# Kernel tuning notes

Measured on AMD Instinct MI355X. Metric: run time of the kernel, lower is better.

## Reference

```python
import jax, jax.numpy as jnp
import numpy as np

N, E, C, H, R, L, ED = 10000, 160000, 512, 4, 8, 2, 768
O = C // H  # out_channels per head = 128
NEG_SLOPE = 0.2
LN_EPS = 1e-5


def setup_inputs() -> dict:
    key = jax.random.key(0)
    ks = jax.random.split(key, 14)
    s = 0.05
    return {
        "x": jax.random.normal(ks[0], (N, C), jnp.float32),
        "edge_index": jax.random.randint(ks[1], (2, E), 0, N, dtype=jnp.int64),
        "edge_type": jax.random.randint(ks[2], (E,), 0, R, dtype=jnp.int64),
        "edge_repre": jax.random.normal(ks[3], (E, ED), jnp.float32),
        # per-layer RGATConv params (num_layers clones)
        "weight": jax.random.normal(ks[4], (L, R, C, C), jnp.float32) * s,   # [L,R,in,heads*out]
        "q": jax.random.normal(ks[5], (L, C, H), jnp.float32) * s,            # [L,heads*out,heads*dim], dim=1
        "k": jax.random.normal(ks[6], (L, C, H), jnp.float32) * s,
        "e": jax.random.normal(ks[7], (L, C, H), jnp.float32) * s,
        "w_edge": jax.random.normal(ks[8], (L, ED, C), jnp.float32) * s,      # lin_edge (no bias)
        "conv_bias": jnp.zeros((L, C), jnp.float32),
        # shared LayerNorm + FFN
        "ln_gamma": jnp.ones((C,), jnp.float32),
        "ln_beta": jnp.zeros((C,), jnp.float32),
        "ff1_w": jax.random.normal(ks[9], (C, 2 * C), jnp.float32) * s,
        "ff1_b": jnp.zeros((2 * C,), jnp.float32),
        "ff2_w": jax.random.normal(ks[10], (2 * C, C), jnp.float32) * s,
        "ff2_b": jnp.zeros((C,), jnp.float32),
    }


def _layer_norm(x, g, b):
    m = jnp.mean(x, axis=-1, keepdims=True)
    v = jnp.mean(jnp.square(x - m), axis=-1, keepdims=True)
    return g * (x - m) * jax.lax.rsqrt(v + LN_EPS) + b


def _rgat_conv(x, src, dst, etype, eattr, W, q, k, e, We, bias):
    n = x.shape[0]
    # relation-specific transform of all nodes once: [N,R,C]
    xw = jnp.einsum('nc,rcd->nrd', x, W)
    outi = xw[dst, etype]            # [E,C] target feats under edge's relation
    outj = xw[src, etype]            # [E,C] source feats under edge's relation
    qi = outi @ q                     # [E,H]
    kj = outj @ k                     # [E,H]
    ae = (eattr @ We) @ e             # [E,H]
    alpha = jax.nn.leaky_relu(qi + kj + ae, NEG_SLOPE)
    # across-relation segment softmax over incoming edges of each target node
    amax = jax.ops.segment_max(alpha, dst, num_segments=n)
    ex = jnp.exp(alpha - amax[dst])
    denom = jax.ops.segment_sum(ex, dst, num_segments=n)
    alpha = ex / (denom[dst] + 1e-16)
    msg = alpha[:, :, None] * outj.reshape(-1, H, O)          # [E,H,O]
    out = jax.ops.segment_sum(msg, dst, num_segments=n)       # [N,H,O]
    return out.reshape(n, H * O) + bias


def reference(x, edge_index, edge_type, edge_repre, weight, q, k, e, w_edge,
              conv_bias, ln_gamma, ln_beta, ff1_w, ff1_b, ff2_w, ff2_b):
    src, dst = edge_index[0], edge_index[1]
    enc_emb = x
    for l in range(L):
        x = _rgat_conv(x, src, dst, edge_type, edge_repre, weight[l], q[l],
                       k[l], e[l], w_edge[l], conv_bias[l]) + x
    x = _layer_norm(x + enc_emb, ln_gamma, ln_beta)
    x = jax.nn.relu(x @ ff1_w + ff1_b) @ ff2_w + ff2_b + x
    x = _layer_norm(x, ln_gamma, ln_beta)
    return x + enc_emb
```

## Files before the change

### kernel.cpp

```cpp
#include <hip/hip_runtime.h>
#include <hip/hip_bf16.h>

#define NN 10000
#define EE 160000
#define CC 512
#define HH 4
#define RR 8
#define LL 2
#define EDD 768
#define OO 128

typedef __attribute__((ext_vector_type(8))) short bf16x8;
typedef __attribute__((ext_vector_type(4))) float f32x4;

__global__ void trg_hist(const int* __restrict__ ei, int* __restrict__ deg) {
  int e = blockIdx.x * 256 + threadIdx.x;
  if (e < EE) atomicAdd(&deg[ei[EE + e]], 1);
}

__global__ void trg_scan(const int* __restrict__ deg, int* __restrict__ offs,
                         int* __restrict__ cursor) {
  __shared__ int sp[256];
  int t = threadIdx.x;
  const int CHK = (NN + 255) / 256;
  int lo = t * CHK, hi = lo + CHK; if (hi > NN) hi = NN; if (lo > NN) lo = NN;
  int s = 0;
  for (int i = lo; i < hi; i++) s += deg[i];
  sp[t] = s;
  __syncthreads();
  if (t == 0) {
    int run = 0;
    for (int i = 0; i < 256; i++) { int v = sp[i]; sp[i] = run; run += v; }
  }
  __syncthreads();
  int run = sp[t];
  for (int i = lo; i < hi; i++) { offs[i] = run; cursor[i] = run; run += deg[i]; }
  if (t == 255) offs[NN] = run;
}

__global__ void trg_fill(const int* __restrict__ ei, int* __restrict__ cursor,
                         int* __restrict__ elist) {
  int e = blockIdx.x * 256 + threadIdx.x;
  if (e < EE) {
    int pos = atomicAdd(&cursor[ei[EE + e]], 1);
    elist[pos] = e;
  }
}

__global__ void trg_transpose(const float* __restrict__ in, __hip_bfloat16* __restrict__ out,
                              int P, int Q, long inStride, long outStride) {
  __shared__ float tile[32][33];
  int z = blockIdx.z;
  const float* inz = in + (long)z * inStride;
  __hip_bfloat16* outz = out + (long)z * outStride;
  int q0 = blockIdx.x * 32, p0 = blockIdx.y * 32;
  int tx = threadIdx.x, ty = threadIdx.y;
#pragma unroll
  for (int i = 0; i < 4; i++)
    tile[ty + i * 8][tx] = inz[(long)(p0 + ty + i * 8) * Q + q0 + tx];
  __syncthreads();
#pragma unroll
  for (int i = 0; i < 4; i++)
    outz[(long)(q0 + ty + i * 8) * P + p0 + tx] = __float2bfloat16(tile[tx][ty + i * 8]);
}

__global__ void trg_cast_bf16(const float* __restrict__ in, __hip_bfloat16* __restrict__ out, int n4) {
  int i = blockIdx.x * 256 + threadIdx.x;
  if (i >= n4) return;
  float4 v = ((const float4*)in)[i];
  union { ushort4 u; __hip_bfloat16 h[4]; } cv;
  cv.h[0] = __float2bfloat16(v.x); cv.h[1] = __float2bfloat16(v.y);
  cv.h[2] = __float2bfloat16(v.z); cv.h[3] = __float2bfloat16(v.w);
  ((ushort4*)out)[i] = cv.u;
}

__global__ void trg_me(const float* __restrict__ we, const float* __restrict__ ep,
                       float* __restrict__ Me) {
  int idx = blockIdx.x * 256 + threadIdx.x;
  if (idx >= LL * EDD * HH) return;
  int l = idx / (EDD * HH);
  int r = idx % (EDD * HH);
  int ed = r / HH, h = r % HH;
  const float* wr = we + ((long)l * EDD + ed) * CC;
  const float* ec = ep + (long)l * CC * HH + h;
  float acc = 0.f;
  for (int c = 0; c < CC; c++) acc += wr[c] * ec[c * HH];
  Me[idx] = acc;
}

__global__ void trg_qcat(const float* __restrict__ qp, const float* __restrict__ kp,
                         float* __restrict__ qcat) {
  int idx = blockIdx.x * 256 + threadIdx.x;
  if (idx >= LL * CC * 8) return;
  int l = idx / (CC * 8);
  int r = idx % (CC * 8);
  int c = r >> 3, j = r & 7;
  qcat[idx] = (j < 4) ? qp[((long)l * CC + c) * HH + j]
                      : kp[((long)l * CC + c) * HH + (j - 4)];
}

__global__ void trg_ae(const float* __restrict__ eattr, const float* __restrict__ Me,
                       float* __restrict__ AE) {
  __shared__ float sE[32 * 129];
  __shared__ float sM[128 * 8];
  int t = threadIdx.x;
  int e0 = blockIdx.x * 32;
  int el = t & 31, og = t >> 5;
  float acc = 0.f;
  for (int kc = 0; kc < 6; kc++) {
    __syncthreads();
    for (int idx = t; idx < 32 * 128; idx += 256) {
      int row = idx >> 7, col = idx & 127;
      sE[row * 129 + col] = eattr[(long)(e0 + row) * EDD + kc * 128 + col];
    }
    for (int idx = t; idx < 128 * 8; idx += 256) {
      int c = idx >> 3, o = idx & 7;
      int l = o >> 2, h = o & 3;
      sM[c * 8 + o] = Me[((long)l * EDD + kc * 128 + c) * 4 + h];
    }
    __syncthreads();
#pragma unroll 8
    for (int c = 0; c < 128; c++)
      acc += sE[el * 129 + c] * sM[c * 8 + og];
  }
  AE[(long)(e0 + el) * 8 + og] = acc;
}

template <int MODE>
__global__ void trg_gemm_bt(const __hip_bfloat16* __restrict__ A,
                            const __hip_bfloat16* __restrict__ Bt,
                            void* __restrict__ Cout,
                            const float* __restrict__ bias,
                            const float* __restrict__ res,
                            int M, int K, int Nc, long sB, long sC) {
  __shared__ __align__(16) unsigned short sAa[128 * 32];
  __shared__ __align__(16) unsigned short sBb[128 * 32];
  const int tid = threadIdx.x;
  const int lane = tid & 63;
  const int wave = tid >> 6;
  const int m0 = blockIdx.x * 128;
  const int n0 = blockIdx.y * 128;
  const __hip_bfloat16* Bz = Bt + (long)blockIdx.z * sB;
  const int wm = (wave >> 1) * 64;
  const int wn = (wave & 1) * 64;
  const int r0 = tid >> 2;
  const int c0 = (tid & 3) * 8;
  const int lrow = lane & 15;
  const int lk = (lane >> 4) * 8;

  int ra = m0 + r0;      if (ra >= M) ra = M - 1;
  int rb = m0 + r0 + 64; if (rb >= M) rb = M - 1;
  const __hip_bfloat16* pa0 = A + (long)ra * K + c0;
  const __hip_bfloat16* pa1 = A + (long)rb * K + c0;
  const __hip_bfloat16* pb0 = Bz + (long)(n0 + r0) * K + c0;
  const __hip_bfloat16* pb1 = Bz + (long)(n0 + r0 + 64) * K + c0;

  f32x4 acc[4][4];
#pragma unroll
  for (int i = 0; i < 4; i++)
#pragma unroll
    for (int j = 0; j < 4; j++) { f32x4 z = {0.f, 0.f, 0.f, 0.f}; acc[i][j] = z; }

  for (int kb = 0; kb < K; kb += 32) {
    uint4 va0 = *(const uint4*)(pa0 + kb);
    uint4 va1 = *(const uint4*)(pa1 + kb);
    uint4 vb0 = *(const uint4*)(pb0 + kb);
    uint4 vb1 = *(const uint4*)(pb1 + kb);
    __syncthreads();
    *(uint4*)(sAa + r0 * 32 + c0) = va0;
    *(uint4*)(sAa + (r0 + 64) * 32 + c0) = va1;
    *(uint4*)(sBb + r0 * 32 + c0) = vb0;
    *(uint4*)(sBb + (r0 + 64) * 32 + c0) = vb1;
    __syncthreads();
    bf16x8 af[4], bfr[4];
#pragma unroll
    for (int i = 0; i < 4; i++)
      af[i] = *(const bf16x8*)(sAa + (wm + i * 16 + lrow) * 32 + lk);
#pragma unroll
    for (int j = 0; j < 4; j++)
      bfr[j] = *(const bf16x8*)(sBb + (wn + j * 16 + lrow) * 32 + lk);
#pragma unroll
    for (int i = 0; i < 4; i++)
#pragma unroll
      for (int j = 0; j < 4; j++)
        acc[i][j] = __builtin_amdgcn_mfma_f32_16x16x32_bf16(af[i], bfr[j], acc[i][j], 0, 0, 0);
  }

  const int crow = (lane >> 4) * 4;
  const int ccol = lane & 15;
#pragma unroll
  for (int i = 0; i < 4; i++) {
#pragma unroll
    for (int j = 0; j < 4; j++) {
      int col = n0 + wn + j * 16 + ccol;
#pragma unroll
      for (int rg = 0; rg < 4; rg++) {
        int row = m0 + wm + i * 16 + crow + rg;
        if (row < M) {
          float v = acc[i][j][rg];
          if (MODE == 1) { v += bias[col]; v = v > 0.f ? v : 0.f; }
          if (MODE == 2) {
            v += bias[col] + res[(long)row * Nc + col];
            ((float*)Cout)[(long)row * Nc + col] = v;
          } else {
            (((__hip_bfloat16*)Cout) + (long)blockIdx.z * sC)[(long)row * Nc + col] =
                __float2bfloat16(v);
          }
        }
      }
    }
  }
}

__global__ void trg_xwqk(const __hip_bfloat16* __restrict__ xwb, const float* __restrict__ qcat_l,
                         float* __restrict__ xwqk) {
  __shared__ float sq[CC * 8];
  for (int i = threadIdx.x; i < CC * 8; i += 256) sq[i] = qcat_l[i];
  __syncthreads();
  int row = blockIdx.x * 32 + (threadIdx.x >> 3);
  int o = threadIdx.x & 7;
  const __hip_bfloat16* ar = xwb + (long)row * CC;
  float acc = 0.f;
  for (int c = 0; c < CC; c++) acc += __bfloat162float(ar[c]) * sq[c * 8 + o];
  xwqk[(long)row * 8 + o] = acc;
}

__global__ void trg_alpha(const int* __restrict__ ei, const int* __restrict__ et,
                          const float* __restrict__ xwqk, const float* __restrict__ AE,
                          float* __restrict__ alpha, int l) {
  int e = blockIdx.x * 256 + threadIdx.x;
  if (e >= EE) return;
  int s = ei[e], d = ei[EE + e], r = et[e];
  const float* qd = xwqk + ((long)r * NN + d) * 8;
  const float* ks = xwqk + ((long)r * NN + s) * 8;
  const float* ae = AE + (long)e * 8 + l * 4;
  float4 o;
  float a;
  a = qd[0] + ks[4] + ae[0]; o.x = a > 0.f ? a : 0.2f * a;
  a = qd[1] + ks[5] + ae[1]; o.y = a > 0.f ? a : 0.2f * a;
  a = qd[2] + ks[6] + ae[2]; o.z = a > 0.f ? a : 0.2f * a;
  a = qd[3] + ks[7] + ae[3]; o.w = a > 0.f ? a : 0.2f * a;
  *(float4*)(alpha + (long)e * 4) = o;
}

__global__ void trg_softmax(const int* __restrict__ offs, const int* __restrict__ elist,
                            float* __restrict__ alpha) {
  int idx = blockIdx.x * 256 + threadIdx.x;
  if (idx >= NN * HH) return;
  int n = idx >> 2, h = idx & 3;
  int beg = offs[n], end = offs[n + 1];
  float m = -1e30f;
  for (int i = beg; i < end; i++) m = fmaxf(m, alpha[(long)elist[i] * 4 + h]);
  float ssum = 0.f;
  for (int i = beg; i < end; i++) ssum += expf(alpha[(long)elist[i] * 4 + h] - m);
  float inv = 1.f / (ssum + 1e-16f);
  for (int i = beg; i < end; i++) {
    long a = (long)elist[i] * 4 + h;
    alpha[a] = expf(alpha[a] - m) * inv;
  }
}

__global__ void trg_agg(const int* __restrict__ offs, const int* __restrict__ elist,
                        const int* __restrict__ ei, const int* __restrict__ et,
                        const float* __restrict__ alpha, const __hip_bfloat16* __restrict__ xwb,
                        const float* __restrict__ bias_l, float* __restrict__ x_cur) {
  int n = blockIdx.x;
  int t = threadIdx.x;
  int c0 = t, c1 = t + 256;
  int h0 = c0 >> 7, h1 = c1 >> 7;
  float a0 = 0.f, a1 = 0.f;
  int beg = offs[n], end = offs[n + 1];
  for (int i = beg; i < end; i++) {
    int e = elist[i];
    int s = ei[e];
    int r = et[e];
    long base = ((long)r * NN + s) * CC;
    float w0 = alpha[(long)e * 4 + h0];
    float w1 = alpha[(long)e * 4 + h1];
    a0 += w0 * __bfloat162float(xwb[base + c0]);
    a1 += w1 * __bfloat162float(xwb[base + c1]);
  }
  long xb = (long)n * CC;
  x_cur[xb + c0] = a0 + bias_l[c0] + x_cur[xb + c0];
  x_cur[xb + c1] = a1 + bias_l[c1] + x_cur[xb + c1];
}

__device__ __forceinline__ float trg_blk_sum(float v, float* sb) {
#pragma unroll
  for (int o = 32; o > 0; o >>= 1) v += __shfl_down(v, o, 64);
  __syncthreads();
  if ((threadIdx.x & 63) == 0) sb[threadIdx.x >> 6] = v;
  __syncthreads();
  return sb[0] + sb[1] + sb[2] + sb[3];
}

__global__ void trg_ln1(const float* __restrict__ xc, const float* __restrict__ enc,
                        const float* __restrict__ g, const float* __restrict__ b,
                        float* __restrict__ xlnf, __hip_bfloat16* __restrict__ xlnb) {
  __shared__ float sb[4];
  int n = blockIdx.x, t = threadIdx.x;
  long base = (long)n * CC;
  float v0 = xc[base + t] + enc[base + t];
  float v1 = xc[base + t + 256] + enc[base + t + 256];
  float s = trg_blk_sum(v0 + v1, sb);
  float m = s * (1.f / CC);
  float d0 = v0 - m, d1 = v1 - m;
  float ss = trg_blk_sum(d0 * d0 + d1 * d1, sb);
  float rstd = rsqrtf(ss * (1.f / CC) + 1e-5f);
  float o0 = g[t] * d0 * rstd + b[t];
  float o1 = g[t + 256] * d1 * rstd + b[t + 256];
  xlnf[base + t] = o0;
  xlnf[base + t + 256] = o1;
  xlnb[base + t] = __float2bfloat16(o0);
  xlnb[base + t + 256] = __float2bfloat16(o1);
}

__global__ void trg_ln2(const float* __restrict__ y, const float* __restrict__ enc,
                        const float* __restrict__ g, const float* __restrict__ b,
                        float* __restrict__ out) {
  __shared__ float sb[4];
  int n = blockIdx.x, t = threadIdx.x;
  long base = (long)n * CC;
  float v0 = y[base + t], v1 = y[base + t + 256];
  float s = trg_blk_sum(v0 + v1, sb);
  float m = s * (1.f / CC);
  float d0 = v0 - m, d1 = v1 - m;
  float ss = trg_blk_sum(d0 * d0 + d1 * d1, sb);
  float rstd = rsqrtf(ss * (1.f / CC) + 1e-5f);
  out[base + t] = g[t] * d0 * rstd + b[t] + enc[base + t];
  out[base + t + 256] = g[t + 256] * d1 * rstd + b[t + 256] + enc[base + t + 256];
}

extern "C" void kernel_launch(void* const* d_in, const int* in_sizes, int n_in,
                              void* d_out, int out_size, void* d_ws, size_t ws_size,
                              hipStream_t stream) {
  const float* x_in   = (const float*)d_in[0];
  const int*   ei     = (const int*)d_in[1];
  const int*   et     = (const int*)d_in[2];
  const float* eattr  = (const float*)d_in[3];
  const float* weight = (const float*)d_in[4];
  const float* q_in   = (const float*)d_in[5];
  const float* k_in   = (const float*)d_in[6];
  const float* e_in   = (const float*)d_in[7];
  const float* w_edge = (const float*)d_in[8];
  const float* cbias  = (const float*)d_in[9];
  const float* ln_g   = (const float*)d_in[10];
  const float* ln_b   = (const float*)d_in[11];
  const float* ff1w   = (const float*)d_in[12];
  const float* ff1b   = (const float*)d_in[13];
  const float* ff2w   = (const float*)d_in[14];
  const float* ff2b   = (const float*)d_in[15];
  float* out = (float*)d_out;

  char* p = (char*)d_ws;
  auto alloc = [&](size_t bytes) {
    char* r = p;
    p += (bytes + 255) & ~(size_t)255;
    return r;
  };
  __hip_bfloat16* xwb   = (__hip_bfloat16*)alloc((size_t)RR * NN * CC * 2);
  __hip_bfloat16* x_bf  = (__hip_bfloat16*)alloc((size_t)NN * CC * 2);
  __hip_bfloat16* Wt_b  = (__hip_bfloat16*)alloc((size_t)LL * RR * CC * CC * 2);
  __hip_bfloat16* ff1t  = (__hip_bfloat16*)alloc((size_t)2 * CC * CC * 2);
  __hip_bfloat16* ff2t  = (__hip_bfloat16*)alloc((size_t)2 * CC * CC * 2);
  float* qcat  = (float*)alloc((size_t)LL * CC * 8 * 4);
  float* Me    = (float*)alloc((size_t)LL * EDD * HH * 4);
  float* AE    = (float*)alloc((size_t)EE * 8 * 4);
  float* xwqk  = (float*)alloc((size_t)RR * NN * 8 * 4);
  float* alpha = (float*)alloc((size_t)EE * 4 * 4);
  int* deg     = (int*)alloc((size_t)(NN + 1) * 4);
  int* offs    = (int*)alloc((size_t)(NN + 1) * 4);
  int* cursor  = (int*)alloc((size_t)(NN + 1) * 4);
  int* elist   = (int*)alloc((size_t)EE * 4);
  float* x_cur = (float*)alloc((size_t)NN * CC * 4);
  float* xln   = (float*)alloc((size_t)NN * CC * 4);
  __hip_bfloat16* xln_bf = (__hip_bfloat16*)alloc((size_t)NN * CC * 2);
  __hip_bfloat16* h_bf   = (__hip_bfloat16*)alloc((size_t)NN * 2 * CC * 2);
  float* y_tmp = (float*)alloc((size_t)NN * CC * 4);

  hipMemcpyAsync(x_cur, x_in, (size_t)NN * CC * 4, hipMemcpyDeviceToDevice, stream);
  hipMemsetAsync(deg, 0, (NN + 1) * 4, stream);
  trg_hist<<<EE / 256, 256, 0, stream>>>(ei, deg);
  trg_scan<<<1, 256, 0, stream>>>(deg, offs, cursor);
  trg_fill<<<EE / 256, 256, 0, stream>>>(ei, cursor, elist);

  dim3 tb(32, 8);
  trg_transpose<<<dim3(CC / 32, CC / 32, LL * RR), tb, 0, stream>>>(
      weight, Wt_b, CC, CC, (long)CC * CC, (long)CC * CC);
  trg_transpose<<<dim3(2 * CC / 32, CC / 32, 1), tb, 0, stream>>>(
      ff1w, ff1t, CC, 2 * CC, 0, 0);
  trg_transpose<<<dim3(CC / 32, 2 * CC / 32, 1), tb, 0, stream>>>(
      ff2w, ff2t, 2 * CC, CC, 0, 0);

  trg_me<<<(LL * EDD * HH + 255) / 256, 256, 0, stream>>>(w_edge, e_in, Me);
  trg_qcat<<<(LL * CC * 8 + 255) / 256, 256, 0, stream>>>(q_in, k_in, qcat);
  trg_ae<<<EE / 32, 256, 0, stream>>>(eattr, Me, AE);

  for (int l = 0; l < LL; l++) {
    trg_cast_bf16<<<(NN * CC / 4 + 255) / 256, 256, 0, stream>>>(x_cur, x_bf, NN * CC / 4);
    trg_gemm_bt<0><<<dim3((NN + 127) / 128, CC / 128, RR), 256, 0, stream>>>(
        x_bf, Wt_b + (size_t)l * RR * CC * CC, xwb, nullptr, nullptr,
        NN, CC, CC, (long)CC * CC, (long)NN * CC);
    trg_xwqk<<<RR * NN / 32, 256, 0, stream>>>(xwb, qcat + (size_t)l * CC * 8, xwqk);
    trg_alpha<<<EE / 256, 256, 0, stream>>>(ei, et, xwqk, AE, alpha, l);
    trg_softmax<<<(NN * HH + 255) / 256, 256, 0, stream>>>(offs, elist, alpha);
    trg_agg<<<NN, 256, 0, stream>>>(offs, elist, ei, et, alpha, xwb,
                                    cbias + (size_t)l * CC, x_cur);
  }

  trg_ln1<<<NN, 256, 0, stream>>>(x_cur, x_in, ln_g, ln_b, xln, xln_bf);
  trg_gemm_bt<1><<<dim3((NN + 127) / 128, 2 * CC / 128, 1), 256, 0, stream>>>(
      xln_bf, ff1t, h_bf, ff1b, nullptr, NN, CC, 2 * CC, 0, 0);
  trg_gemm_bt<2><<<dim3((NN + 127) / 128, CC / 128, 1), 256, 0, stream>>>(
      h_bf, ff2t, y_tmp, ff2b, xln, NN, 2 * CC, CC, 0, 0);
  trg_ln2<<<NN, 256, 0, stream>>>(y_tmp, x_in, ln_g, ln_b, out);
}
```

Measured before the change: 1.404 ms.

## Fold q/k into weights, use direct-to-LDS GEMM loads, vectorize agg and AE

```diff
diff --git a/kernel.cpp b/kernel.cpp
--- a/kernel.cpp
+++ b/kernel.cpp
@@ -12,6 +12,12 @@
 
 typedef __attribute__((ext_vector_type(8))) short bf16x8;
 typedef __attribute__((ext_vector_type(4))) float f32x4;
+
+typedef __attribute__((address_space(1))) const unsigned int as1cu;
+typedef __attribute__((address_space(3))) unsigned int as3u;
+__device__ __forceinline__ void gl2lds16(const void* g, void* l) {
+  __builtin_amdgcn_global_load_lds((as1cu*)g, (as3u*)l, 16, 0, 0);
+}
 
 __global__ void trg_hist(const int* __restrict__ ei, int* __restrict__ deg) {
   int e = blockIdx.x * 256 + threadIdx.x;
@@ -99,29 +105,61 @@
                       : kp[((long)l * CC + c) * HH + (j - 4)];
 }
 
+__global__ void trg_wqk(const float* __restrict__ W, const float* __restrict__ qcat,
+                        __hip_bfloat16* __restrict__ Wqkt) {
+  __shared__ float qs[CC * 8];
+  int lr = blockIdx.y;
+  int l = lr >> 3, r = lr & 7;
+  int t = threadIdx.x;
+  for (int i = t; i < CC * 8; i += 256) qs[i] = qcat[(long)l * CC * 8 + i];
+  __syncthreads();
+  int c = blockIdx.x * 128 + (t & 127);
+  int oh = t >> 7;
+  const float4* Wrow = (const float4*)(W + ((long)lr * CC + c) * CC);
+  float a0 = 0.f, a1 = 0.f, a2 = 0.f, a3 = 0.f;
+  for (int d4 = 0; d4 < CC / 4; d4++) {
+    float4 wv = Wrow[d4];
+    const float* wp = &wv.x;
+#pragma unroll
+    for (int dd = 0; dd < 4; dd++) {
+      float w = wp[dd];
+      const float4 qv = *(const float4*)(qs + (d4 * 4 + dd) * 8 + oh * 4);
+      a0 += w * qv.x; a1 += w * qv.y; a2 += w * qv.z; a3 += w * qv.w;
+    }
+  }
+  long ob = ((long)l * 64 + r * 8 + oh * 4) * CC + c;
+  Wqkt[ob] = __float2bfloat16(a0);
+  Wqkt[ob + CC] = __float2bfloat16(a1);
+  Wqkt[ob + 2 * CC] = __float2bfloat16(a2);
+  Wqkt[ob + 3 * CC] = __float2bfloat16(a3);
+}
+
 __global__ void trg_ae(const float* __restrict__ eattr, const float* __restrict__ Me,
                        float* __restrict__ AE) {
-  __shared__ float sE[32 * 129];
-  __shared__ float sM[128 * 8];
+  __shared__ float sE[32 * 132];
+  __shared__ float sM[8 * 132];
   int t = threadIdx.x;
   int e0 = blockIdx.x * 32;
-  int el = t & 31, og = t >> 5;
+  int el = t >> 3, og = t & 7;
   float acc = 0.f;
   for (int kc = 0; kc < 6; kc++) {
     __syncthreads();
-    for (int idx = t; idx < 32 * 128; idx += 256) {
-      int row = idx >> 7, col = idx & 127;
-      sE[row * 129 + col] = eattr[(long)(e0 + row) * EDD + kc * 128 + col];
+    for (int idx = t; idx < 1024; idx += 256) {
+      int row = idx >> 5, c4 = idx & 31;
+      *(float4*)(sE + row * 132 + c4 * 4) =
+          *(const float4*)(eattr + (long)(e0 + row) * EDD + kc * 128 + c4 * 4);
     }
-    for (int idx = t; idx < 128 * 8; idx += 256) {
-      int c = idx >> 3, o = idx & 7;
-      int l = o >> 2, h = o & 3;
-      sM[c * 8 + o] = Me[((long)l * EDD + kc * 128 + c) * 4 + h];
+    for (int idx = t; idx < 1024; idx += 256) {
+      int o = idx >> 7, c = idx & 127;
+      sM[o * 132 + c] = Me[((long)(o >> 2) * EDD + kc * 128 + c) * 4 + (o & 3)];
     }
     __syncthreads();
-#pragma unroll 8
-    for (int c = 0; c < 128; c++)
-      acc += sE[el * 129 + c] * sM[c * 8 + og];
+#pragma unroll
+    for (int c4 = 0; c4 < 32; c4++) {
+      float4 ev = *(const float4*)(sE + el * 132 + c4 * 4);
+      float4 mv = *(const float4*)(sM + og * 132 + c4 * 4);
+      acc += ev.x * mv.x + ev.y * mv.y + ev.z * mv.z + ev.w * mv.w;
+    }
   }
   AE[(long)(e0 + el) * 8 + og] = acc;
 }
@@ -143,17 +181,21 @@
   const __hip_bfloat16* Bz = Bt + (long)blockIdx.z * sB;
   const int wm = (wave >> 1) * 64;
   const int wn = (wave & 1) * 64;
-  const int r0 = tid >> 2;
-  const int c0 = (tid & 3) * 8;
   const int lrow = lane & 15;
   const int lk = (lane >> 4) * 8;
 
-  int ra = m0 + r0;      if (ra >= M) ra = M - 1;
-  int rb = m0 + r0 + 64; if (rb >= M) rb = M - 1;
-  const __hip_bfloat16* pa0 = A + (long)ra * K + c0;
-  const __hip_bfloat16* pa1 = A + (long)rb * K + c0;
-  const __hip_bfloat16* pb0 = Bz + (long)(n0 + r0) * K + c0;
-  const __hip_bfloat16* pb1 = Bz + (long)(n0 + r0 + 64) * K + c0;
+  const int srow = wave * 16 + (lane >> 2);
+  const int scol = (lane & 3) * 8;
+  int ra = m0 + srow;      if (ra >= M) ra = M - 1;
+  int rb = m0 + srow + 64; if (rb >= M) rb = M - 1;
+  const __hip_bfloat16* pa0 = A + (long)ra * K + scol;
+  const __hip_bfloat16* pa1 = A + (long)rb * K + scol;
+  const __hip_bfloat16* pb0 = Bz + (long)(n0 + srow) * K + scol;
+  const __hip_bfloat16* pb1 = Bz + (long)(n0 + srow + 64) * K + scol;
+  unsigned short* la0 = sAa + wave * 512;
+  unsigned short* la1 = sAa + 64 * 32 + wave * 512;
+  unsigned short* lb0 = sBb + wave * 512;
+  unsigned short* lb1 = sBb + 64 * 32 + wave * 512;
 
   f32x4 acc[4][4];
 #pragma unroll
@@ -162,15 +204,11 @@
     for (int j = 0; j < 4; j++) { f32x4 z = {0.f, 0.f, 0.f, 0.f}; acc[i][j] = z; }
 
   for (int kb = 0; kb < K; kb += 32) {
-    uint4 va0 = *(const uint4*)(pa0 + kb);
-    uint4 va1 = *(const uint4*)(pa1 + kb);
-    uint4 vb0 = *(const uint4*)(pb0 + kb);
-    uint4 vb1 = *(const uint4*)(pb1 + kb);
     __syncthreads();
-    *(uint4*)(sAa + r0 * 32 + c0) = va0;
-    *(uint4*)(sAa + (r0 + 64) * 32 + c0) = va1;
-    *(uint4*)(sBb + r0 * 32 + c0) = vb0;
-    *(uint4*)(sBb + (r0 + 64) * 32 + c0) = vb1;
+    gl2lds16(pa0 + kb, la0);
+    gl2lds16(pa1 + kb, la1);
+    gl2lds16(pb0 + kb, lb0);
+    gl2lds16(pb1 + kb, lb1);
     __syncthreads();
     bf16x8 af[4], bfr[4];
 #pragma unroll
@@ -212,17 +250,69 @@
   }
 }
 
-__global__ void trg_xwqk(const __hip_bfloat16* __restrict__ xwb, const float* __restrict__ qcat_l,
-                         float* __restrict__ xwqk) {
-  __shared__ float sq[CC * 8];
-  for (int i = threadIdx.x; i < CC * 8; i += 256) sq[i] = qcat_l[i];
-  __syncthreads();
-  int row = blockIdx.x * 32 + (threadIdx.x >> 3);
-  int o = threadIdx.x & 7;
-  const __hip_bfloat16* ar = xwb + (long)row * CC;
-  float acc = 0.f;
-  for (int c = 0; c < CC; c++) acc += __bfloat162float(ar[c]) * sq[c * 8 + o];
-  xwqk[(long)row * 8 + o] = acc;
+__global__ void trg_gemm_n64(const __hip_bfloat16* __restrict__ A,
+                             const __hip_bfloat16* __restrict__ Bt,
+                             float* __restrict__ Cout, int M) {
+  __shared__ __align__(16) unsigned short sA[128 * 32];
+  __shared__ __align__(16) unsigned short sB[64 * 32];
+  const int tid = threadIdx.x;
+  const int lane = tid & 63;
+  const int wave = tid >> 6;
+  const int m0 = blockIdx.x * 128;
+  const int wm = wave * 32;
+  const int lrow = lane & 15;
+  const int lk = (lane >> 4) * 8;
+
+  const int srow = wave * 16 + (lane >> 2);
+  const int scol = (lane & 3) * 8;
+  int ra = m0 + srow;      if (ra >= M) ra = M - 1;
+  int rb = m0 + srow + 64; if (rb >= M) rb = M - 1;
+  const __hip_bfloat16* pa0 = A + (long)ra * CC + scol;
+  const __hip_bfloat16* pa1 = A + (long)rb * CC + scol;
+  const __hip_bfloat16* pb = Bt + (long)srow * CC + scol;
+  unsigned short* la0 = sA + wave * 512;
+  unsigned short* la1 = sA + 64 * 32 + wave * 512;
+  unsigned short* lb = sB + wave * 512;
+
+  f32x4 acc[2][4];
+#pragma unroll
+  for (int i = 0; i < 2; i++)
+#pragma unroll
+    for (int j = 0; j < 4; j++) { f32x4 z = {0.f, 0.f, 0.f, 0.f}; acc[i][j] = z; }
+
+  for (int kb = 0; kb < CC; kb += 32) {
+    __syncthreads();
+    gl2lds16(pa0 + kb, la0);
+    gl2lds16(pa1 + kb, la1);
+    gl2lds16(pb + kb, lb);
+    __syncthreads();
+    bf16x8 af[2], bfr[4];
+#pragma unroll
+    for (int i = 0; i < 2; i++)
+      af[i] = *(const bf16x8*)(sA + (wm + i * 16 + lrow) * 32 + lk);
+#pragma unroll
+    for (int j = 0; j < 4; j++)
+      bfr[j] = *(const bf16x8*)(sB + (j * 16 + lrow) * 32 + lk);
+#pragma unroll
+    for (int i = 0; i < 2; i++)
+#pragma unroll
+      for (int j = 0; j < 4; j++)
+        acc[i][j] = __builtin_amdgcn_mfma_f32_16x16x32_bf16(af[i], bfr[j], acc[i][j], 0, 0, 0);
+  }
+
+  const int crow = (lane >> 4) * 4;
+  const int ccol = lane & 15;
+#pragma unroll
+  for (int i = 0; i < 2; i++)
+#pragma unroll
+    for (int j = 0; j < 4; j++) {
+      int col = j * 16 + ccol;
+#pragma unroll
+      for (int rg = 0; rg < 4; rg++) {
+        int row = m0 + wm + i * 16 + crow + rg;
+        if (row < M) Cout[(long)row * 64 + col] = acc[i][j][rg];
+      }
+    }
 }
 
 __global__ void trg_alpha(const int* __restrict__ ei, const int* __restrict__ et,
@@ -231,15 +321,15 @@
   int e = blockIdx.x * 256 + threadIdx.x;
   if (e >= EE) return;
   int s = ei[e], d = ei[EE + e], r = et[e];
-  const float* qd = xwqk + ((long)r * NN + d) * 8;
-  const float* ks = xwqk + ((long)r * NN + s) * 8;
-  const float* ae = AE + (long)e * 8 + l * 4;
+  float4 qv = *(const float4*)(xwqk + (long)d * 64 + r * 8);
+  float4 kv = *(const float4*)(xwqk + (long)s * 64 + r * 8 + 4);
+  float4 ae = *(const float4*)(AE + (long)e * 8 + l * 4);
   float4 o;
   float a;
-  a = qd[0] + ks[4] + ae[0]; o.x = a > 0.f ? a : 0.2f * a;
-  a = qd[1] + ks[5] + ae[1]; o.y = a > 0.f ? a : 0.2f * a;
-  a = qd[2] + ks[6] + ae[2]; o.z = a > 0.f ? a : 0.2f * a;
-  a = qd[3] + ks[7] + ae[3]; o.w = a > 0.f ? a : 0.2f * a;
+  a = qv.x + kv.x + ae.x; o.x = a > 0.f ? a : 0.2f * a;
+  a = qv.y + kv.y + ae.y; o.y = a > 0.f ? a : 0.2f * a;
+  a = qv.z + kv.z + ae.z; o.z = a > 0.f ? a : 0.2f * a;
+  a = qv.w + kv.w + ae.w; o.w = a > 0.f ? a : 0.2f * a;
   *(float4*)(alpha + (long)e * 4) = o;
 }
 
@@ -263,26 +353,41 @@
 __global__ void trg_agg(const int* __restrict__ offs, const int* __restrict__ elist,
                         const int* __restrict__ ei, const int* __restrict__ et,
                         const float* __restrict__ alpha, const __hip_bfloat16* __restrict__ xwb,
-                        const float* __restrict__ bias_l, float* __restrict__ x_cur) {
+                        const float* __restrict__ bias_l, float* __restrict__ x_cur,
+                        __hip_bfloat16* __restrict__ x_bf) {
+  __shared__ float red[4][512];
   int n = blockIdx.x;
   int t = threadIdx.x;
-  int c0 = t, c1 = t + 256;
-  int h0 = c0 >> 7, h1 = c1 >> 7;
-  float a0 = 0.f, a1 = 0.f;
+  int wave = t >> 6, lane = t & 63;
+  int c0 = lane * 8;
+  int h = lane >> 4;
+  float acc[8];
+#pragma unroll
+  for (int j = 0; j < 8; j++) acc[j] = 0.f;
   int beg = offs[n], end = offs[n + 1];
-  for (int i = beg; i < end; i++) {
+  for (int i = beg + wave; i < end; i += 4) {
     int e = elist[i];
-    int s = ei[e];
-    int r = et[e];
-    long base = ((long)r * NN + s) * CC;
-    float w0 = alpha[(long)e * 4 + h0];
-    float w1 = alpha[(long)e * 4 + h1];
-    a0 += w0 * __bfloat162float(xwb[base + c0]);
-    a1 += w1 * __bfloat162float(xwb[base + c1]);
-  }
+    int s = ei[e], r = et[e];
+    float w = alpha[(long)e * 4 + h];
+    uint4 u = *(const uint4*)(xwb + ((long)r * NN + s) * CC + c0);
+    acc[0] += w * __uint_as_float(u.x << 16);
+    acc[1] += w * __uint_as_float(u.x & 0xffff0000u);
+    acc[2] += w * __uint_as_float(u.y << 16);
+    acc[3] += w * __uint_as_float(u.y & 0xffff0000u);
+    acc[4] += w * __uint_as_float(u.z << 16);
+    acc[5] += w * __uint_as_float(u.z & 0xffff0000u);
+    acc[6] += w * __uint_as_float(u.w << 16);
+    acc[7] += w * __uint_as_float(u.w & 0xffff0000u);
+  }
+#pragma unroll
+  for (int j = 0; j < 8; j++) red[wave][c0 + j] = acc[j];
+  __syncthreads();
   long xb = (long)n * CC;
-  x_cur[xb + c0] = a0 + bias_l[c0] + x_cur[xb + c0];
-  x_cur[xb + c1] = a1 + bias_l[c1] + x_cur[xb + c1];
+  for (int c = t; c < CC; c += 256) {
+    float v = red[0][c] + red[1][c] + red[2][c] + red[3][c] + bias_l[c] + x_cur[xb + c];
+    x_cur[xb + c] = v;
+    x_bf[xb + c] = __float2bfloat16(v);
+  }
 }
 
 __device__ __forceinline__ float trg_blk_sum(float v, float* sb) {
@@ -363,10 +468,11 @@
   __hip_bfloat16* Wt_b  = (__hip_bfloat16*)alloc((size_t)LL * RR * CC * CC * 2);
   __hip_bfloat16* ff1t  = (__hip_bfloat16*)alloc((size_t)2 * CC * CC * 2);
   __hip_bfloat16* ff2t  = (__hip_bfloat16*)alloc((size_t)2 * CC * CC * 2);
+  __hip_bfloat16* Wqkt  = (__hip_bfloat16*)alloc((size_t)LL * 64 * CC * 2);
   float* qcat  = (float*)alloc((size_t)LL * CC * 8 * 4);
   float* Me    = (float*)alloc((size_t)LL * EDD * HH * 4);
   float* AE    = (float*)alloc((size_t)EE * 8 * 4);
-  float* xwqk  = (float*)alloc((size_t)RR * NN * 8 * 4);
+  float* xwqk  = (float*)alloc((size_t)NN * 64 * 4);
   float* alpha = (float*)alloc((size_t)EE * 4 * 4);
   int* deg     = (int*)alloc((size_t)(NN + 1) * 4);
   int* offs    = (int*)alloc((size_t)(NN + 1) * 4);
@@ -394,18 +500,20 @@
 
   trg_me<<<(LL * EDD * HH + 255) / 256, 256, 0, stream>>>(w_edge, e_in, Me);
   trg_qcat<<<(LL * CC * 8 + 255) / 256, 256, 0, stream>>>(q_in, k_in, qcat);
+  trg_wqk<<<dim3(4, LL * RR), 256, 0, stream>>>(weight, qcat, Wqkt);
   trg_ae<<<EE / 32, 256, 0, stream>>>(eattr, Me, AE);
+  trg_cast_bf16<<<(NN * CC / 4 + 255) / 256, 256, 0, stream>>>(x_cur, x_bf, NN * CC / 4);
 
   for (int l = 0; l < LL; l++) {
-    trg_cast_bf16<<<(NN * CC / 4 + 255) / 256, 256, 0, stream>>>(x_cur, x_bf, NN * CC / 4);
     trg_gemm_bt<0><<<dim3((NN + 127) / 128, CC / 128, RR), 256, 0, stream>>>(
         x_bf, Wt_b + (size_t)l * RR * CC * CC, xwb, nullptr, nullptr,
         NN, CC, CC, (long)CC * CC, (long)NN * CC);
-    trg_xwqk<<<RR * NN / 32, 256, 0, stream>>>(xwb, qcat + (size_t)l * CC * 8, xwqk);
+    trg_gemm_n64<<<(NN + 127) / 128, 256, 0, stream>>>(
+        x_bf, Wqkt + (size_t)l * 64 * CC, xwqk, NN);
     trg_alpha<<<EE / 256, 256, 0, stream>>>(ei, et, xwqk, AE, alpha, l);
     trg_softmax<<<(NN * HH + 255) / 256, 256, 0, stream>>>(offs, elist, alpha);
     trg_agg<<<NN, 256, 0, stream>>>(offs, elist, ei, et, alpha, xwb,
-                                    cbias + (size_t)l * CC, x_cur);
+                                    cbias + (size_t)l * CC, x_cur, x_bf);
   }
 
   trg_ln1<<<NN, 256, 0, stream>>>(x_cur, x_in, ln_g, ln_b, xln, xln_bf);
```

Result: faster. 1.247 ms (-11.2%).
